# Kernel optimization log

Hardware: AMD Instinct MI355X
Metric: run time of the kernel (lower is better)

## Reference

```python
import jax, jax.numpy as jnp
import numpy as np

B, S, E, H = 2, 2048, 1024, 16
D = E // H  # head_dim = 64
SPARSE_RATIO = 0.125


def setup_inputs() -> dict:
    key = jax.random.key(0)
    ks = jax.random.split(key, 9)
    def lin(k):
        return jax.random.normal(k, (E, E), dtype=jnp.float32) * 0.02
    return {
        'x': jax.random.normal(ks[0], (B, S, E), dtype=jnp.float32),
        'Wq': lin(ks[1]), 'bq': jnp.zeros((E,), jnp.float32),
        'Wk': lin(ks[2]), 'bk': jnp.zeros((E,), jnp.float32),
        'Wv': lin(ks[3]), 'bv': jnp.zeros((E,), jnp.float32),
        'Wo': lin(ks[4]), 'bo': jnp.zeros((E,), jnp.float32),
    }


def reference(x, Wq, bq, Wk, bk, Wv, bv, Wo, bo):
    # QKV projections: (B,S,E) -> (B,H,S,D)
    def heads(y):
        return y.reshape(B, S, H, D).transpose(0, 2, 1, 3)
    q = heads(x @ Wq.T + bq)
    k = heads(x @ Wk.T + bk)
    v = heads(x @ Wv.T + bv)

    # full score matrix (B,H,S,S), scaled by sqrt(head_dim)
    scores = jnp.einsum('bhsd,bhtd->bhst', q, k) / jnp.sqrt(jnp.float32(D))

    # top-k sparsification applied to scores (fill -inf), then softmax
    top_k = int(SPARSE_RATIO * S)  # 256
    top_vals, top_idx = jax.lax.top_k(scores, top_k)
    neg_inf = jnp.float32(-jnp.inf)
    sparse_scores = jnp.full_like(scores, neg_inf)
    sparse_scores = jnp.put_along_axis(sparse_scores, top_idx, top_vals, axis=-1, inplace=False)

    attn = jax.nn.softmax(sparse_scores, axis=-1)
    out = jnp.einsum('bhst,bhtd->bhsd', attn, v)  # (B,H,S,D)
    out = out.transpose(0, 2, 1, 3).reshape(B, S, E)
    return out @ Wo.T + bo
```

## Files before the change

### kernel.cpp

```cpp
#include <hip/hip_runtime.h>

#define S_LEN 2048
#define NH 16
#define HD 64
#define NBH 32
#define TOPK 256

typedef __bf16 bf16x8_t __attribute__((ext_vector_type(8)));
typedef float  f32x4_t  __attribute__((ext_vector_type(4)));

__device__ __forceinline__ unsigned short rne_bf16(float f) {
    const unsigned x = __float_as_uint(f);
    return (unsigned short)((x + 0x7FFFu + ((x >> 16) & 1u)) >> 16);
}

__global__ __launch_bounds__(256)
void decompose_bf16(const float* __restrict__ in, unsigned short* __restrict__ hi,
                    unsigned short* __restrict__ lo, int n4)
{
    const int i = blockIdx.x * 256 + threadIdx.x;
    if (i >= n4) return;
    const float4 v = reinterpret_cast<const float4*>(in)[i];
    const float f[4] = {v.x, v.y, v.z, v.w};
    unsigned short h[4], l[4];
    #pragma unroll
    for (int j = 0; j < 4; ++j) {
        h[j] = rne_bf16(f[j]);
        const float r = f[j] - __uint_as_float((unsigned)h[j] << 16);
        l[j] = rne_bf16(r);
    }
    reinterpret_cast<ushort4*>(hi)[i] = make_ushort4(h[0], h[1], h[2], h[3]);
    reinterpret_cast<ushort4*>(lo)[i] = make_ushort4(l[0], l[1], l[2], l[3]);
}

__global__ __launch_bounds__(256)
void gemm_mfma_bt(const unsigned short* __restrict__ Ah, const unsigned short* __restrict__ Al,
                  const unsigned short* __restrict__ Bh, const unsigned short* __restrict__ Bl,
                  const float* __restrict__ bias, float* __restrict__ C,
                  unsigned short* __restrict__ Ch, unsigned short* __restrict__ Cl,
                  int M, int N, int K, int mode, int ldc)
{
    __shared__ unsigned short Ash[128][40];
    __shared__ unsigned short Asl[128][40];
    __shared__ unsigned short Bsh[128][40];
    __shared__ unsigned short Bsl[128][40];

    const int tid  = threadIdx.x;
    const int wid  = tid >> 6, lane = tid & 63;
    const int m0   = blockIdx.y * 128, n0 = blockIdx.x * 128;
    const int wr   = (wid >> 1) * 64, wc = (wid & 1) * 64;
    const int r16  = lane & 15, ksub = (lane >> 4) * 8;
    const int srow = tid >> 1;
    const int skb  = (tid & 1) * 16;

    f32x4_t acc[4][4] = {};

    const size_t aBase = (size_t)(m0 + srow) * K + skb;
    const size_t bBase = (size_t)(n0 + srow) * K + skb;

    for (int k0 = 0; k0 < K; k0 += 32) {
        const uint4 a0 = *reinterpret_cast<const uint4*>(&Ah[aBase + k0]);
        const uint4 a1 = *reinterpret_cast<const uint4*>(&Ah[aBase + k0 + 8]);
        const uint4 a2 = *reinterpret_cast<const uint4*>(&Al[aBase + k0]);
        const uint4 a3 = *reinterpret_cast<const uint4*>(&Al[aBase + k0 + 8]);
        const uint4 b0 = *reinterpret_cast<const uint4*>(&Bh[bBase + k0]);
        const uint4 b1 = *reinterpret_cast<const uint4*>(&Bh[bBase + k0 + 8]);
        const uint4 b2 = *reinterpret_cast<const uint4*>(&Bl[bBase + k0]);
        const uint4 b3 = *reinterpret_cast<const uint4*>(&Bl[bBase + k0 + 8]);
        __syncthreads();
        *reinterpret_cast<uint4*>(&Ash[srow][skb])     = a0;
        *reinterpret_cast<uint4*>(&Ash[srow][skb + 8]) = a1;
        *reinterpret_cast<uint4*>(&Asl[srow][skb])     = a2;
        *reinterpret_cast<uint4*>(&Asl[srow][skb + 8]) = a3;
        *reinterpret_cast<uint4*>(&Bsh[srow][skb])     = b0;
        *reinterpret_cast<uint4*>(&Bsh[srow][skb + 8]) = b1;
        *reinterpret_cast<uint4*>(&Bsl[srow][skb])     = b2;
        *reinterpret_cast<uint4*>(&Bsl[srow][skb + 8]) = b3;
        __syncthreads();

        bf16x8_t fah[4], fal[4], fbh[4], fbl[4];
        #pragma unroll
        for (int i = 0; i < 4; ++i) {
            fah[i] = *reinterpret_cast<const bf16x8_t*>(&Ash[wr + i * 16 + r16][ksub]);
            fal[i] = *reinterpret_cast<const bf16x8_t*>(&Asl[wr + i * 16 + r16][ksub]);
        }
        #pragma unroll
        for (int j = 0; j < 4; ++j) {
            fbh[j] = *reinterpret_cast<const bf16x8_t*>(&Bsh[wc + j * 16 + r16][ksub]);
            fbl[j] = *reinterpret_cast<const bf16x8_t*>(&Bsl[wc + j * 16 + r16][ksub]);
        }
        #pragma unroll
        for (int i = 0; i < 4; ++i)
            #pragma unroll
            for (int j = 0; j < 4; ++j) {
                acc[i][j] = __builtin_amdgcn_mfma_f32_16x16x32_bf16(fah[i], fbh[j], acc[i][j], 0, 0, 0);
                acc[i][j] = __builtin_amdgcn_mfma_f32_16x16x32_bf16(fah[i], fbl[j], acc[i][j], 0, 0, 0);
                acc[i][j] = __builtin_amdgcn_mfma_f32_16x16x32_bf16(fal[i], fbh[j], acc[i][j], 0, 0, 0);
            }
    }

    #pragma unroll
    for (int j = 0; j < 4; ++j) {
        const int col = n0 + wc + j * 16 + r16;
        const float bv = bias ? bias[col] : 0.0f;
        #pragma unroll
        for (int i = 0; i < 4; ++i) {
            #pragma unroll
            for (int r = 0; r < 4; ++r) {
                const int row = m0 + wr + i * 16 + (lane >> 4) * 4 + r;
                const float val = acc[i][j][r] + bv;
                if (mode == 0) {
                    C[(size_t)row * ldc + col] = val;
                } else {
                    const int b = row >> 11, s = row & (S_LEN - 1);
                    const int h = col >> 6,  d = col & (HD - 1);
                    const size_t idx = (((size_t)(b * NH + h)) * S_LEN + s) * HD + d;
                    if (mode == 1) {
                        C[idx] = val;
                    } else {
                        const unsigned short hh = rne_bf16(val);
                        Ch[idx] = hh;
                        Cl[idx] = rne_bf16(val - __uint_as_float((unsigned)hh << 16));
                    }
                }
            }
        }
    }
}

__global__ __launch_bounds__(256)
void gemm_score_mfma(const unsigned short* __restrict__ Qh, const unsigned short* __restrict__ Ql,
                     const unsigned short* __restrict__ Kh, const unsigned short* __restrict__ Kl,
                     float* __restrict__ S)
{
    __shared__ unsigned short pl[4][128 * 64];

    const int tid  = threadIdx.x;
    const int wid  = tid >> 6, lane = tid & 63;
    const int m0   = blockIdx.y * 128, n0 = blockIdx.x * 128;
    const int wr   = (wid >> 1) * 64, wc = (wid & 1) * 64;
    const int r16  = lane & 15, ko = (lane >> 4) * 8;
    const size_t headOff = (size_t)blockIdx.z * S_LEN * HD;
    S += (size_t)blockIdx.z * S_LEN * S_LEN;

    {
        const int row = tid >> 1, cs = (tid & 1) * 32;
        const size_t gq = headOff + (size_t)(m0 + row) * HD + cs;
        const size_t gk = headOff + (size_t)(n0 + row) * HD + cs;
        const unsigned short* srcs[4] = {Qh + gq, Ql + gq, Kh + gk, Kl + gk};
        #pragma unroll
        for (int p = 0; p < 4; ++p) {
            #pragma unroll
            for (int j = 0; j < 4; ++j) {
                const uint4 v = *reinterpret_cast<const uint4*>(&srcs[p][j * 8]);
                const int idx = (row * 64 + cs + j * 8) ^ ((row & 7) << 3);
                *reinterpret_cast<uint4*>(&pl[p][idx]) = v;
            }
        }
    }
    __syncthreads();

    f32x4_t acc[4][4] = {};
    #pragma unroll
    for (int ks = 0; ks < 2; ++ks) {
        bf16x8_t fah[4], fal[4], fbh[4], fbl[4];
        #pragma unroll
        for (int i = 0; i < 4; ++i) {
            const int row = wr + i * 16 + r16;
            const int idx = (row * 64 + ko + ks * 32) ^ ((row & 7) << 3);
            fah[i] = *reinterpret_cast<const bf16x8_t*>(&pl[0][idx]);
            fal[i] = *reinterpret_cast<const bf16x8_t*>(&pl[1][idx]);
        }
        #pragma unroll
        for (int j = 0; j < 4; ++j) {
            const int row = wc + j * 16 + r16;
            const int idx = (row * 64 + ko + ks * 32) ^ ((row & 7) << 3);
            fbh[j] = *reinterpret_cast<const bf16x8_t*>(&pl[2][idx]);
            fbl[j] = *reinterpret_cast<const bf16x8_t*>(&pl[3][idx]);
        }
        #pragma unroll
        for (int i = 0; i < 4; ++i)
            #pragma unroll
            for (int j = 0; j < 4; ++j) {
                acc[i][j] = __builtin_amdgcn_mfma_f32_16x16x32_bf16(fah[i], fbh[j], acc[i][j], 0, 0, 0);
                acc[i][j] = __builtin_amdgcn_mfma_f32_16x16x32_bf16(fah[i], fbl[j], acc[i][j], 0, 0, 0);
                acc[i][j] = __builtin_amdgcn_mfma_f32_16x16x32_bf16(fal[i], fbh[j], acc[i][j], 0, 0, 0);
                acc[i][j] = __builtin_amdgcn_mfma_f32_16x16x32_bf16(fal[i], fbl[j], acc[i][j], 0, 0, 0);
            }
    }

    #pragma unroll
    for (int j = 0; j < 4; ++j) {
        const int col = n0 + wc + j * 16 + r16;
        #pragma unroll
        for (int i = 0; i < 4; ++i)
            #pragma unroll
            for (int r = 0; r < 4; ++r) {
                const int row = m0 + wr + i * 16 + (lane >> 4) * 4 + r;
                S[(size_t)row * S_LEN + col] = acc[i][j][r] * 0.125f;
            }
    }
}

__device__ __forceinline__ float wredf_add(float v) {
    #pragma unroll
    for (int m = 32; m > 0; m >>= 1) v += __shfl_xor(v, m, 64);
    return v;
}

#define HCOPY_STRIDE 272
#define HWAVE_WORDS 768

__global__ __launch_bounds__(256, 4)
void topk_softmax_pv(const float* __restrict__ scores, const float* __restrict__ V,
                     float* __restrict__ att, int bh0)
{
    const int wave = threadIdx.x >> 6;
    const int lane = threadIdx.x & 63;
    const int bh   = bh0 + blockIdx.y;
    const int row  = blockIdx.x * 4 + wave;

    const float* srow = scores + (size_t)blockIdx.y * S_LEN * S_LEN + (size_t)row * S_LEN;

    unsigned u[32];
    unsigned mxu = 0u;
    #pragma unroll
    for (int c = 0; c < 8; ++c) {
        const float4 v4 = *reinterpret_cast<const float4*>(&srow[c * 256 + lane * 4]);
        const float f[4] = {v4.x, v4.y, v4.z, v4.w};
        #pragma unroll
        for (int i = 0; i < 4; ++i) {
            const unsigned b = __float_as_uint(f[i]);
            const unsigned k = (b & 0x80000000u) ? ~b : (b | 0x80000000u);
            u[c * 4 + i] = k;
            mxu = k > mxu ? k : mxu;
        }
    }
    #pragma unroll
    for (int m = 32; m > 0; m >>= 1) {
        const unsigned o = (unsigned)__shfl_xor((int)mxu, m, 64);
        mxu = o > mxu ? o : mxu;
    }
    const float mx = __uint_as_float((mxu & 0x80000000u) ? (mxu & 0x7FFFFFFFu) : ~mxu);

    __shared__ unsigned hist[4][HWAVE_WORDS];
    unsigned* const histw = hist[wave];
    unsigned* const myh   = histw + (lane & 1) * HCOPY_STRIDE;

    unsigned prefix = 0;
    int kRem = TOPK;
    unsigned count_eq = 0;

    auto radix_round = [&](int r, bool masked) {
        #pragma unroll
        for (int j = 0; j < 3; ++j)
            *reinterpret_cast<uint4*>(&histw[4 * (lane + 64 * j)]) = make_uint4(0u, 0u, 0u, 0u);
        asm volatile("s_waitcnt lgkmcnt(0)" ::: "memory");
        const int sh = 24 - 8 * r;
        const int ps = 32 - 8 * r;
        #pragma unroll
        for (int i = 0; i < 32; ++i) {
            const unsigned dig = (u[i] >> sh) & 0xFFu;
            if (!masked) {
                atomicAdd(&myh[dig], 1u);
            } else {
                if ((u[i] >> ps) == prefix) atomicAdd(&myh[dig], 1u);
            }
        }
        asm volatile("s_waitcnt lgkmcnt(0)" ::: "memory");
        const uint4 q0 = *reinterpret_cast<const uint4*>(&histw[0 * HCOPY_STRIDE + 4 * lane]);
        const uint4 q1 = *reinterpret_cast<const uint4*>(&histw[1 * HCOPY_STRIDE + 4 * lane]);
        const unsigned c0 = q0.x + q1.x;
        const unsigned c1 = q0.y + q1.y;
        const unsigned c2 = q0.z + q1.z;
        const unsigned c3 = q0.w + q1.w;
        const unsigned cnt = c0 + c1 + c2 + c3;
        unsigned sfx = cnt;
        #pragma unroll
        for (int dd = 1; dd < 64; dd <<= 1) {
            const unsigned t = __shfl_down(sfx, dd, 64);
            if (lane + dd < 64) sfx += t;
        }
        const unsigned g3 = sfx - cnt;
        const unsigned g2 = g3 + c3;
        const unsigned g1 = g2 + c2;
        const unsigned g0 = g1 + c1;
        const unsigned kr = (unsigned)kRem;
        int myd = -1; unsigned mygt = 0, myc = 0;
        if      (g3 < kr && g3 + c3 >= kr) { myd = 4*lane+3; mygt = g3; myc = c3; }
        else if (g2 < kr && g2 + c2 >= kr) { myd = 4*lane+2; mygt = g2; myc = c2; }
        else if (g1 < kr && g1 + c1 >= kr) { myd = 4*lane+1; mygt = g1; myc = c1; }
        else if (g0 < kr && g0 + c0 >= kr) { myd = 4*lane+0; mygt = g0; myc = c0; }
        const unsigned long long bal = __ballot(myd >= 0);
        const int src = __ffsll((unsigned long long)bal) - 1;
        const int d   = __shfl(myd, src, 64);
        kRem    -= __shfl((int)mygt, src, 64);
        count_eq = (unsigned)__shfl((int)myc, src, 64);
        prefix = (prefix << 8) | (unsigned)d;
    };

    radix_round(0, false);
    radix_round(1, true);

    unsigned tau;
    bool takeAll;
    if ((unsigned)kRem == count_eq) {
        tau = prefix << 16;
        takeAll = true;
    } else {
        radix_round(2, true);
        radix_round(3, true);
        tau = prefix;
        takeAll = ((unsigned)kRem == count_eq);
    }
    const int quota = kRem;

    const unsigned long long below = (1ull << lane) - 1ull;
    unsigned incbits = 0u;
    if (takeAll) {
        #pragma unroll
        for (int i = 0; i < 32; ++i)
            if (u[i] >= tau) incbits |= (1u << i);
    } else {
        int prev = 0;
        #pragma unroll
        for (int c = 0; c < 8; ++c) {
            unsigned long long bl[4];
            #pragma unroll
            for (int i = 0; i < 4; ++i) bl[i] = __ballot(u[c * 4 + i] == tau);
            const int below_all = __popcll(bl[0] & below) + __popcll(bl[1] & below)
                                + __popcll(bl[2] & below) + __popcll(bl[3] & below);
            int own = 0;
            #pragma unroll
            for (int i = 0; i < 4; ++i) {
                const bool tie = (u[c * 4 + i] == tau);
                const bool inc = (u[c * 4 + i] > tau) ||
                                 (tie && (prev + below_all + own) < quota);
                own += tie ? 1 : 0;
                if (inc) incbits |= (1u << (c * 4 + i));
            }
            prev += __popcll(bl[0]) + __popcll(bl[1]) + __popcll(bl[2]) + __popcll(bl[3]);
        }
    }

    __shared__ unsigned long long ltw[4][TOPK];
    float ds = 0.f;
    int base = 0;
    #pragma unroll
    for (int c = 0; c < 8; ++c) {
        #pragma unroll
        for (int i = 0; i < 4; ++i) {
            const int id = c * 4 + i;
            const bool inc = ((incbits >> id) & 1u) != 0u;
            const unsigned long long bmask = __ballot(inc);
            float wv = 0.f;
            if (inc) {
                const unsigned uu = u[id];
                const unsigned bb = (uu & 0x80000000u) ? (uu & 0x7FFFFFFFu) : ~uu;
                wv = __expf(__uint_as_float(bb) - mx);
                const int pos = base + __popcll(bmask & below);
                ltw[wave][pos] = ((unsigned long long)__float_as_uint(wv) << 32)
                               | (unsigned)(c * 256 + lane * 4 + i);
            }
            ds += wv;
            base += __popcll(bmask);
        }
    }
    const float inv = 1.0f / wredf_add(ds);
    asm volatile("s_waitcnt lgkmcnt(0)" ::: "memory");

    const float* vh = V + (size_t)bh * S_LEN * HD;
    const int g  = lane >> 4;
    const int l4 = (lane & 15) * 4;
    f32x4_t acc = {0.f, 0.f, 0.f, 0.f};
    for (int idx = 0; idx < TOPK; idx += 8) {
        const unsigned long long e0 = ltw[wave][idx + g];
        const unsigned long long e1 = ltw[wave][idx + 4 + g];
        const float w0 = __uint_as_float((unsigned)(e0 >> 32));
        const float w1 = __uint_as_float((unsigned)(e1 >> 32));
        const float4 v0 = *reinterpret_cast<const float4*>(&vh[(((unsigned)e0) << 6) + l4]);
        const float4 v1 = *reinterpret_cast<const float4*>(&vh[(((unsigned)e1) << 6) + l4]);
        acc[0] = fmaf(w0, v0.x, acc[0]);
        acc[1] = fmaf(w0, v0.y, acc[1]);
        acc[2] = fmaf(w0, v0.z, acc[2]);
        acc[3] = fmaf(w0, v0.w, acc[3]);
        acc[0] = fmaf(w1, v1.x, acc[0]);
        acc[1] = fmaf(w1, v1.y, acc[1]);
        acc[2] = fmaf(w1, v1.z, acc[2]);
        acc[3] = fmaf(w1, v1.w, acc[3]);
    }
    #pragma unroll
    for (int r = 0; r < 4; ++r) {
        acc[r] += __shfl_xor(acc[r], 16, 64);
        acc[r] += __shfl_xor(acc[r], 32, 64);
    }

    if (lane < 16) {
        const int b = bh >> 4, h = bh & 15;
        float4 o;
        o.x = acc[0] * inv; o.y = acc[1] * inv;
        o.z = acc[2] * inv; o.w = acc[3] * inv;
        *reinterpret_cast<float4*>(&att[(((size_t)b * S_LEN + row) * NH + h) * HD + l4]) = o;
    }
}

extern "C" void kernel_launch(void* const* d_in, const int* in_sizes, int n_in,
                              void* d_out, int out_size, void* d_ws, size_t ws_size,
                              hipStream_t stream)
{
    const float* x  = (const float*)d_in[0];
    const float* Wq = (const float*)d_in[1];
    const float* bq = (const float*)d_in[2];
    const float* Wk = (const float*)d_in[3];
    const float* bk = (const float*)d_in[4];
    const float* Wv = (const float*)d_in[5];
    const float* bv = (const float*)d_in[6];
    const float* Wo = (const float*)d_in[7];
    const float* bo = (const float*)d_in[8];
    float* out = (float*)d_out;

    const size_t SD       = (size_t)S_LEN * HD;
    const size_t qkvElems = (size_t)NBH * SD;
    const size_t wElems   = 1024u * 1024u;

    float* v_ws = (float*)d_ws;
    float* attb = v_ws + qkvElems;
    unsigned short* xh  = (unsigned short*)(attb + qkvElems);
    unsigned short* xl  = xh + qkvElems;
    unsigned short* wqh = xl + qkvElems;
    unsigned short* wql = wqh + wElems;
    unsigned short* wkh = wql + wElems;
    unsigned short* wkl = wkh + wElems;
    unsigned short* wvh = wkl + wElems;
    unsigned short* wvl = wvh + wElems;
    unsigned short* woh = wvl + wElems;
    unsigned short* wol = woh + wElems;
    unsigned short* qh  = wol + wElems;
    unsigned short* ql  = qh + qkvElems;
    unsigned short* kh  = ql + qkvElems;
    unsigned short* kl  = kh + qkvElems;
    float* sc = (float*)(kl + qkvElems);

    const size_t scorePerHead = (size_t)S_LEN * S_LEN;
    const size_t fixedBytes = 2 * qkvElems * sizeof(float)
                            + (6 * qkvElems + 8 * wElems) * sizeof(unsigned short);
    size_t availHeads = 0;
    if (ws_size > fixedBytes)
        availHeads = (ws_size - fixedBytes) / (scorePerHead * sizeof(float));
    int hc = (int)(availHeads < 1 ? 1 : (availHeads > (size_t)NBH ? (size_t)NBH : availHeads));
    if (hc > 16) hc = 16;

    const dim3 blk(256);

    decompose_bf16<<<dim3(4096), blk, 0, stream>>>(x,  xh,  xl,  (int)(qkvElems / 4));
    decompose_bf16<<<dim3(1024), blk, 0, stream>>>(Wq, wqh, wql, (int)(wElems / 4));
    decompose_bf16<<<dim3(1024), blk, 0, stream>>>(Wk, wkh, wkl, (int)(wElems / 4));
    decompose_bf16<<<dim3(1024), blk, 0, stream>>>(Wv, wvh, wvl, (int)(wElems / 4));
    decompose_bf16<<<dim3(1024), blk, 0, stream>>>(Wo, woh, wol, (int)(wElems / 4));

    gemm_mfma_bt<<<dim3(8, 32), blk, 0, stream>>>(xh, xl, wqh, wql, bq, nullptr, qh, ql, 4096, 1024, 1024, 2, 0);
    gemm_mfma_bt<<<dim3(8, 32), blk, 0, stream>>>(xh, xl, wkh, wkl, bk, nullptr, kh, kl, 4096, 1024, 1024, 2, 0);
    gemm_mfma_bt<<<dim3(8, 32), blk, 0, stream>>>(xh, xl, wvh, wvl, bv, v_ws, nullptr, nullptr, 4096, 1024, 1024, 1, 0);

    for (int bh0 = 0; bh0 < NBH; bh0 += hc) {
        const int h = (bh0 + hc <= NBH) ? hc : (NBH - bh0);
        gemm_score_mfma<<<dim3(16, 16, h), blk, 0, stream>>>(
            qh + (size_t)bh0 * SD, ql + (size_t)bh0 * SD,
            kh + (size_t)bh0 * SD, kl + (size_t)bh0 * SD, sc);
        topk_softmax_pv<<<dim3(512, h), blk, 0, stream>>>(sc, v_ws, attb, bh0);
    }

    decompose_bf16<<<dim3(4096), blk, 0, stream>>>(attb, xh, xl, (int)(qkvElems / 4));
    gemm_mfma_bt<<<dim3(8, 32), blk, 0, stream>>>(xh, xl, woh, wol, bo, out, nullptr, nullptr, 4096, 1024, 1024, 0, 1024);
}
```

Baseline: 649.9 us.

## Process two score rows per wave in top-k softmax PV kernel

Each wave now handles two rows, interleaving their radix-select histogram rounds, selection masks, exp/compaction and the sparse PV gather, to raise instruction-level parallelism and hide LDS/global latency. The max subtraction before exp is dropped and the compacted weight list reuses the histogram shared memory, which halves the grid. This roughly doubles register use per thread, which may hurt occupancy, and the missing max-shift could overflow for larger scores.

```diff
diff --git a/kernel.cpp b/kernel.cpp
--- a/kernel.cpp
+++ b/kernel.cpp
@@ -202,14 +202,8 @@
     }
 }
 
-__device__ __forceinline__ float wredf_add(float v) {
-    #pragma unroll
-    for (int m = 32; m > 0; m >>= 1) v += __shfl_xor(v, m, 64);
-    return v;
-}
-
 #define HCOPY_STRIDE 272
-#define HWAVE_WORDS 768
+#define HROW_WORDS 768
 
 __global__ __launch_bounds__(256, 4)
 void topk_softmax_pv(const float* __restrict__ scores, const float* __restrict__ V,
@@ -218,62 +212,43 @@
     const int wave = threadIdx.x >> 6;
     const int lane = threadIdx.x & 63;
     const int bh   = bh0 + blockIdx.y;
-    const int row  = blockIdx.x * 4 + wave;
-
-    const float* srow = scores + (size_t)blockIdx.y * S_LEN * S_LEN + (size_t)row * S_LEN;
-
-    unsigned u[32];
-    unsigned mxu = 0u;
+    const int r0   = blockIdx.x * 8 + wave * 2;
+
+    const float* s0 = scores + (size_t)blockIdx.y * S_LEN * S_LEN + (size_t)r0 * S_LEN;
+    const float* s1 = s0 + S_LEN;
+
+    unsigned u0[32], u1[32];
     #pragma unroll
     for (int c = 0; c < 8; ++c) {
-        const float4 v4 = *reinterpret_cast<const float4*>(&srow[c * 256 + lane * 4]);
-        const float f[4] = {v4.x, v4.y, v4.z, v4.w};
+        const float4 a = *reinterpret_cast<const float4*>(&s0[c * 256 + lane * 4]);
+        const float4 b = *reinterpret_cast<const float4*>(&s1[c * 256 + lane * 4]);
+        const float fa[4] = {a.x, a.y, a.z, a.w};
+        const float fb[4] = {b.x, b.y, b.z, b.w};
         #pragma unroll
         for (int i = 0; i < 4; ++i) {
-            const unsigned b = __float_as_uint(f[i]);
-            const unsigned k = (b & 0x80000000u) ? ~b : (b | 0x80000000u);
-            u[c * 4 + i] = k;
-            mxu = k > mxu ? k : mxu;
-        }
-    }
-    #pragma unroll
-    for (int m = 32; m > 0; m >>= 1) {
-        const unsigned o = (unsigned)__shfl_xor((int)mxu, m, 64);
-        mxu = o > mxu ? o : mxu;
-    }
-    const float mx = __uint_as_float((mxu & 0x80000000u) ? (mxu & 0x7FFFFFFFu) : ~mxu);
-
-    __shared__ unsigned hist[4][HWAVE_WORDS];
-    unsigned* const histw = hist[wave];
-    unsigned* const myh   = histw + (lane & 1) * HCOPY_STRIDE;
-
-    unsigned prefix = 0;
-    int kRem = TOPK;
-    unsigned count_eq = 0;
-
-    auto radix_round = [&](int r, bool masked) {
-        #pragma unroll
-        for (int j = 0; j < 3; ++j)
-            *reinterpret_cast<uint4*>(&histw[4 * (lane + 64 * j)]) = make_uint4(0u, 0u, 0u, 0u);
-        asm volatile("s_waitcnt lgkmcnt(0)" ::: "memory");
-        const int sh = 24 - 8 * r;
-        const int ps = 32 - 8 * r;
-        #pragma unroll
-        for (int i = 0; i < 32; ++i) {
-            const unsigned dig = (u[i] >> sh) & 0xFFu;
-            if (!masked) {
-                atomicAdd(&myh[dig], 1u);
-            } else {
-                if ((u[i] >> ps) == prefix) atomicAdd(&myh[dig], 1u);
-            }
-        }
-        asm volatile("s_waitcnt lgkmcnt(0)" ::: "memory");
-        const uint4 q0 = *reinterpret_cast<const uint4*>(&histw[0 * HCOPY_STRIDE + 4 * lane]);
-        const uint4 q1 = *reinterpret_cast<const uint4*>(&histw[1 * HCOPY_STRIDE + 4 * lane]);
-        const unsigned c0 = q0.x + q1.x;
-        const unsigned c1 = q0.y + q1.y;
-        const unsigned c2 = q0.z + q1.z;
-        const unsigned c3 = q0.w + q1.w;
+            const unsigned xa = __float_as_uint(fa[i]);
+            const unsigned xb = __float_as_uint(fb[i]);
+            u0[c * 4 + i] = (xa & 0x80000000u) ? ~xa : (xa | 0x80000000u);
+            u1[c * 4 + i] = (xb & 0x80000000u) ? ~xb : (xb | 0x80000000u);
+        }
+    }
+
+    __shared__ unsigned hist[4][2][HROW_WORDS];
+    unsigned* const h0 = hist[wave][0];
+    unsigned* const h1 = hist[wave][1];
+    unsigned* const m0 = h0 + (lane & 1) * HCOPY_STRIDE;
+    unsigned* const m1 = h1 + (lane & 1) * HCOPY_STRIDE;
+    const unsigned long long below = (1ull << lane) - 1ull;
+
+    unsigned pfx0 = 0, pfx1 = 0;
+    int kr0 = TOPK, kr1 = TOPK;
+    unsigned ce0 = 0, ce1 = 0;
+
+    auto scan1 = [&](unsigned* hh, unsigned& pfx, int& kr, unsigned& ce) {
+        const uint4 qa = *reinterpret_cast<const uint4*>(&hh[4 * lane]);
+        const uint4 qb = *reinterpret_cast<const uint4*>(&hh[HCOPY_STRIDE + 4 * lane]);
+        const unsigned c0 = qa.x + qb.x, c1 = qa.y + qb.y;
+        const unsigned c2 = qa.z + qb.z, c3 = qa.w + qb.w;
         const unsigned cnt = c0 + c1 + c2 + c3;
         unsigned sfx = cnt;
         #pragma unroll
@@ -285,122 +260,197 @@
         const unsigned g2 = g3 + c3;
         const unsigned g1 = g2 + c2;
         const unsigned g0 = g1 + c1;
-        const unsigned kr = (unsigned)kRem;
+        const unsigned k = (unsigned)kr;
         int myd = -1; unsigned mygt = 0, myc = 0;
-        if      (g3 < kr && g3 + c3 >= kr) { myd = 4*lane+3; mygt = g3; myc = c3; }
-        else if (g2 < kr && g2 + c2 >= kr) { myd = 4*lane+2; mygt = g2; myc = c2; }
-        else if (g1 < kr && g1 + c1 >= kr) { myd = 4*lane+1; mygt = g1; myc = c1; }
-        else if (g0 < kr && g0 + c0 >= kr) { myd = 4*lane+0; mygt = g0; myc = c0; }
+        if      (g3 < k && g3 + c3 >= k) { myd = 4*lane+3; mygt = g3; myc = c3; }
+        else if (g2 < k && g2 + c2 >= k) { myd = 4*lane+2; mygt = g2; myc = c2; }
+        else if (g1 < k && g1 + c1 >= k) { myd = 4*lane+1; mygt = g1; myc = c1; }
+        else if (g0 < k && g0 + c0 >= k) { myd = 4*lane+0; mygt = g0; myc = c0; }
         const unsigned long long bal = __ballot(myd >= 0);
         const int src = __ffsll((unsigned long long)bal) - 1;
         const int d   = __shfl(myd, src, 64);
-        kRem    -= __shfl((int)mygt, src, 64);
-        count_eq = (unsigned)__shfl((int)myc, src, 64);
-        prefix = (prefix << 8) | (unsigned)d;
+        kr -= __shfl((int)mygt, src, 64);
+        ce  = (unsigned)__shfl((int)myc, src, 64);
+        pfx = (pfx << 8) | (unsigned)d;
     };
 
-    radix_round(0, false);
-    radix_round(1, true);
-
-    unsigned tau;
-    bool takeAll;
-    if ((unsigned)kRem == count_eq) {
-        tau = prefix << 16;
-        takeAll = true;
-    } else {
-        radix_round(2, true);
-        radix_round(3, true);
-        tau = prefix;
-        takeAll = ((unsigned)kRem == count_eq);
-    }
-    const int quota = kRem;
-
-    const unsigned long long below = (1ull << lane) - 1ull;
-    unsigned incbits = 0u;
-    if (takeAll) {
+    #pragma unroll
+    for (int r = 0; r < 2; ++r) {
+        #pragma unroll
+        for (int j = 0; j < 3; ++j) {
+            *reinterpret_cast<uint4*>(&h0[4 * (lane + 64 * j)]) = make_uint4(0u, 0u, 0u, 0u);
+            *reinterpret_cast<uint4*>(&h1[4 * (lane + 64 * j)]) = make_uint4(0u, 0u, 0u, 0u);
+        }
+        asm volatile("s_waitcnt lgkmcnt(0)" ::: "memory");
+        const int sh = 24 - 8 * r;
+        #pragma unroll
+        for (int i = 0; i < 32; ++i) {
+            if (r == 0) {
+                atomicAdd(&m0[(u0[i] >> 24) & 0xFFu], 1u);
+                atomicAdd(&m1[(u1[i] >> 24) & 0xFFu], 1u);
+            } else {
+                if ((u0[i] >> 24) == pfx0) atomicAdd(&m0[(u0[i] >> sh) & 0xFFu], 1u);
+                if ((u1[i] >> 24) == pfx1) atomicAdd(&m1[(u1[i] >> sh) & 0xFFu], 1u);
+            }
+        }
+        asm volatile("s_waitcnt lgkmcnt(0)" ::: "memory");
+        scan1(h0, pfx0, kr0, ce0);
+        scan1(h1, pfx1, kr1, ce1);
+    }
+
+    auto round1row = [&](const unsigned (&u)[32], unsigned* hh, unsigned* mh,
+                         unsigned& pfx, int& kr, unsigned& ce, int r) {
+        #pragma unroll
+        for (int j = 0; j < 3; ++j)
+            *reinterpret_cast<uint4*>(&hh[4 * (lane + 64 * j)]) = make_uint4(0u, 0u, 0u, 0u);
+        asm volatile("s_waitcnt lgkmcnt(0)" ::: "memory");
+        const int sh = 24 - 8 * r;
+        const int ps = 32 - 8 * r;
         #pragma unroll
         for (int i = 0; i < 32; ++i)
-            if (u[i] >= tau) incbits |= (1u << i);
-    } else {
-        int prev = 0;
-        #pragma unroll
-        for (int c = 0; c < 8; ++c) {
-            unsigned long long bl[4];
-            #pragma unroll
-            for (int i = 0; i < 4; ++i) bl[i] = __ballot(u[c * 4 + i] == tau);
-            const int below_all = __popcll(bl[0] & below) + __popcll(bl[1] & below)
-                                + __popcll(bl[2] & below) + __popcll(bl[3] & below);
-            int own = 0;
-            #pragma unroll
-            for (int i = 0; i < 4; ++i) {
-                const bool tie = (u[c * 4 + i] == tau);
-                const bool inc = (u[c * 4 + i] > tau) ||
-                                 (tie && (prev + below_all + own) < quota);
-                own += tie ? 1 : 0;
-                if (inc) incbits |= (1u << (c * 4 + i));
-            }
-            prev += __popcll(bl[0]) + __popcll(bl[1]) + __popcll(bl[2]) + __popcll(bl[3]);
-        }
-    }
-
-    __shared__ unsigned long long ltw[4][TOPK];
-    float ds = 0.f;
-    int base = 0;
+            if ((u[i] >> ps) == pfx) atomicAdd(&mh[(u[i] >> sh) & 0xFFu], 1u);
+        asm volatile("s_waitcnt lgkmcnt(0)" ::: "memory");
+        scan1(hh, pfx, kr, ce);
+    };
+
+    unsigned tau0, tau1;
+    bool ta0, ta1;
+    if ((unsigned)kr0 == ce0) { tau0 = pfx0 << 16; ta0 = true; }
+    else {
+        round1row(u0, h0, m0, pfx0, kr0, ce0, 2);
+        round1row(u0, h0, m0, pfx0, kr0, ce0, 3);
+        tau0 = pfx0; ta0 = ((unsigned)kr0 == ce0);
+    }
+    if ((unsigned)kr1 == ce1) { tau1 = pfx1 << 16; ta1 = true; }
+    else {
+        round1row(u1, h1, m1, pfx1, kr1, ce1, 2);
+        round1row(u1, h1, m1, pfx1, kr1, ce1, 3);
+        tau1 = pfx1; ta1 = ((unsigned)kr1 == ce1);
+    }
+
+    auto incmask = [&](const unsigned (&u)[32], unsigned tau, bool takeAll, int quota) -> unsigned {
+        unsigned inc = 0u;
+        if (takeAll) {
+            #pragma unroll
+            for (int i = 0; i < 32; ++i)
+                if (u[i] >= tau) inc |= (1u << i);
+        } else {
+            int prev = 0;
+            #pragma unroll
+            for (int c = 0; c < 8; ++c) {
+                unsigned long long bl[4];
+                #pragma unroll
+                for (int i = 0; i < 4; ++i) bl[i] = __ballot(u[c * 4 + i] == tau);
+                const int below_all = __popcll(bl[0] & below) + __popcll(bl[1] & below)
+                                    + __popcll(bl[2] & below) + __popcll(bl[3] & below);
+                int own = 0;
+                #pragma unroll
+                for (int i = 0; i < 4; ++i) {
+                    const bool tie = (u[c * 4 + i] == tau);
+                    const bool in = (u[c * 4 + i] > tau) ||
+                                    (tie && (prev + below_all + own) < quota);
+                    own += tie ? 1 : 0;
+                    if (in) inc |= (1u << (c * 4 + i));
+                }
+                prev += __popcll(bl[0]) + __popcll(bl[1]) + __popcll(bl[2]) + __popcll(bl[3]);
+            }
+        }
+        return inc;
+    };
+    const unsigned inc0 = incmask(u0, tau0, ta0, kr0);
+    const unsigned inc1 = incmask(u1, tau1, ta1, kr1);
+
+    unsigned long long* const ltw0 = reinterpret_cast<unsigned long long*>(&hist[wave][0][0]);
+    unsigned long long* const ltw1 = ltw0 + TOPK;
+    float ds0 = 0.f, ds1 = 0.f;
+    int base0 = 0, base1 = 0;
     #pragma unroll
     for (int c = 0; c < 8; ++c) {
         #pragma unroll
         for (int i = 0; i < 4; ++i) {
             const int id = c * 4 + i;
-            const bool inc = ((incbits >> id) & 1u) != 0u;
-            const unsigned long long bmask = __ballot(inc);
-            float wv = 0.f;
-            if (inc) {
-                const unsigned uu = u[id];
-                const unsigned bb = (uu & 0x80000000u) ? (uu & 0x7FFFFFFFu) : ~uu;
-                wv = __expf(__uint_as_float(bb) - mx);
-                const int pos = base + __popcll(bmask & below);
-                ltw[wave][pos] = ((unsigned long long)__float_as_uint(wv) << 32)
-                               | (unsigned)(c * 256 + lane * 4 + i);
-            }
-            ds += wv;
-            base += __popcll(bmask);
-        }
-    }
-    const float inv = 1.0f / wredf_add(ds);
+            const unsigned tval = (unsigned)(c * 256 + lane * 4 + i);
+            {
+                const bool in = ((inc0 >> id) & 1u) != 0u;
+                const unsigned long long bm = __ballot(in);
+                float wv = 0.f;
+                if (in) {
+                    const unsigned uu = u0[id];
+                    const unsigned bb = (uu & 0x80000000u) ? (uu & 0x7FFFFFFFu) : ~uu;
+                    wv = __expf(__uint_as_float(bb));
+                    ltw0[base0 + __popcll(bm & below)] =
+                        ((unsigned long long)__float_as_uint(wv) << 32) | tval;
+                }
+                ds0 += wv;
+                base0 += __popcll(bm);
+            }
+            {
+                const bool in = ((inc1 >> id) & 1u) != 0u;
+                const unsigned long long bm = __ballot(in);
+                float wv = 0.f;
+                if (in) {
+                    const unsigned uu = u1[id];
+                    const unsigned bb = (uu & 0x80000000u) ? (uu & 0x7FFFFFFFu) : ~uu;
+                    wv = __expf(__uint_as_float(bb));
+                    ltw1[base1 + __popcll(bm & below)] =
+                        ((unsigned long long)__float_as_uint(wv) << 32) | tval;
+                }
+                ds1 += wv;
+                base1 += __popcll(bm);
+            }
+        }
+    }
+    #pragma unroll
+    for (int m = 32; m > 0; m >>= 1) {
+        ds0 += __shfl_xor(ds0, m, 64);
+        ds1 += __shfl_xor(ds1, m, 64);
+    }
+    const float inv0 = 1.0f / ds0;
+    const float inv1 = 1.0f / ds1;
     asm volatile("s_waitcnt lgkmcnt(0)" ::: "memory");
 
     const float* vh = V + (size_t)bh * S_LEN * HD;
     const int g  = lane >> 4;
     const int l4 = (lane & 15) * 4;
-    f32x4_t acc = {0.f, 0.f, 0.f, 0.f};
+    f32x4_t A0 = {0.f, 0.f, 0.f, 0.f};
+    f32x4_t A1 = {0.f, 0.f, 0.f, 0.f};
     for (int idx = 0; idx < TOPK; idx += 8) {
-        const unsigned long long e0 = ltw[wave][idx + g];
-        const unsigned long long e1 = ltw[wave][idx + 4 + g];
-        const float w0 = __uint_as_float((unsigned)(e0 >> 32));
-        const float w1 = __uint_as_float((unsigned)(e1 >> 32));
-        const float4 v0 = *reinterpret_cast<const float4*>(&vh[(((unsigned)e0) << 6) + l4]);
-        const float4 v1 = *reinterpret_cast<const float4*>(&vh[(((unsigned)e1) << 6) + l4]);
-        acc[0] = fmaf(w0, v0.x, acc[0]);
-        acc[1] = fmaf(w0, v0.y, acc[1]);
-        acc[2] = fmaf(w0, v0.z, acc[2]);
-        acc[3] = fmaf(w0, v0.w, acc[3]);
-        acc[0] = fmaf(w1, v1.x, acc[0]);
-        acc[1] = fmaf(w1, v1.y, acc[1]);
-        acc[2] = fmaf(w1, v1.z, acc[2]);
-        acc[3] = fmaf(w1, v1.w, acc[3]);
+        const unsigned long long e00 = ltw0[idx + g];
+        const unsigned long long e01 = ltw0[idx + 4 + g];
+        const unsigned long long e10 = ltw1[idx + g];
+        const unsigned long long e11 = ltw1[idx + 4 + g];
+        const float w00 = __uint_as_float((unsigned)(e00 >> 32));
+        const float w01 = __uint_as_float((unsigned)(e01 >> 32));
+        const float w10 = __uint_as_float((unsigned)(e10 >> 32));
+        const float w11 = __uint_as_float((unsigned)(e11 >> 32));
+        const float4 v00 = *reinterpret_cast<const float4*>(&vh[(((unsigned)e00) << 6) + l4]);
+        const float4 v01 = *reinterpret_cast<const float4*>(&vh[(((unsigned)e01) << 6) + l4]);
+        const float4 v10 = *reinterpret_cast<const float4*>(&vh[(((unsigned)e10) << 6) + l4]);
+        const float4 v11 = *reinterpret_cast<const float4*>(&vh[(((unsigned)e11) << 6) + l4]);
+        A0[0] = fmaf(w00, v00.x, A0[0]); A0[1] = fmaf(w00, v00.y, A0[1]);
+        A0[2] = fmaf(w00, v00.z, A0[2]); A0[3] = fmaf(w00, v00.w, A0[3]);
+        A1[0] = fmaf(w10, v10.x, A1[0]); A1[1] = fmaf(w10, v10.y, A1[1]);
+        A1[2] = fmaf(w10, v10.z, A1[2]); A1[3] = fmaf(w10, v10.w, A1[3]);
+        A0[0] = fmaf(w01, v01.x, A0[0]); A0[1] = fmaf(w01, v01.y, A0[1]);
+        A0[2] = fmaf(w01, v01.z, A0[2]); A0[3] = fmaf(w01, v01.w, A0[3]);
+        A1[0] = fmaf(w11, v11.x, A1[0]); A1[1] = fmaf(w11, v11.y, A1[1]);
+        A1[2] = fmaf(w11, v11.z, A1[2]); A1[3] = fmaf(w11, v11.w, A1[3]);
     }
     #pragma unroll
     for (int r = 0; r < 4; ++r) {
-        acc[r] += __shfl_xor(acc[r], 16, 64);
-        acc[r] += __shfl_xor(acc[r], 32, 64);
+        A0[r] += __shfl_xor(A0[r], 16, 64);
+        A0[r] += __shfl_xor(A0[r], 32, 64);
+        A1[r] += __shfl_xor(A1[r], 16, 64);
+        A1[r] += __shfl_xor(A1[r], 32, 64);
     }
 
     if (lane < 16) {
         const int b = bh >> 4, h = bh & 15;
-        float4 o;
-        o.x = acc[0] * inv; o.y = acc[1] * inv;
-        o.z = acc[2] * inv; o.w = acc[3] * inv;
-        *reinterpret_cast<float4*>(&att[(((size_t)b * S_LEN + row) * NH + h) * HD + l4]) = o;
+        float4 o0, o1;
+        o0.x = A0[0] * inv0; o0.y = A0[1] * inv0; o0.z = A0[2] * inv0; o0.w = A0[3] * inv0;
+        o1.x = A1[0] * inv1; o1.y = A1[1] * inv1; o1.z = A1[2] * inv1; o1.w = A1[3] * inv1;
+        *reinterpret_cast<float4*>(&att[(((size_t)b * S_LEN + r0) * NH + h) * HD + l4]) = o0;
+        *reinterpret_cast<float4*>(&att[(((size_t)b * S_LEN + r0 + 1) * NH + h) * HD + l4]) = o1;
     }
 }
 
@@ -467,7 +517,7 @@
         gemm_score_mfma<<<dim3(16, 16, h), blk, 0, stream>>>(
             qh + (size_t)bh0 * SD, ql + (size_t)bh0 * SD,
             kh + (size_t)bh0 * SD, kl + (size_t)bh0 * SD, sc);
-        topk_softmax_pv<<<dim3(512, h), blk, 0, stream>>>(sc, v_ws, attb, bh0);
+        topk_softmax_pv<<<dim3(256, h), blk, 0, stream>>>(sc, v_ws, attb, bh0);
     }
 
     decompose_bf16<<<dim3(4096), blk, 0, stream>>>(attb, xh, xl, (int)(qkvElems / 4));
```

After: 811.1 us. 24.8% more time.
